# Kernel tuning notes

Measured on AMD Instinct MI355X. Metric: run time of the kernel, lower is better.

## Reference

```python
import jax, jax.numpy as jnp
import numpy as np

B, N, E = 4, 160, 200000
D_EDGE, D_ORI, D_TYPE = 128, 8, 120      # d_edge, d_ori_edge, d_edge_type = d_edge - d_ori_edge
D_EXT = 512                               # d_edge * expansion_factor(4)
D_H4 = 512                                # d_edge * 4
D_REL = 16
PML, ETN = 32, 16                         # path_max_length, edge_type_num


def setup_inputs() -> dict:
    key = jax.random.key(0)
    ks = jax.random.split(key, 16)
    p = lambda i, shape, s=0.05: (jax.random.normal(ks[i], shape) * s).astype(jnp.float32)
    return dict(
        rel_type=jax.random.randint(ks[0], (E,), 0, ETN),
        rel_error=jax.random.normal(ks[1], (E, D_ORI), jnp.float32),
        edge_pos=jax.random.randint(ks[2], (E,), 0, PML),
        dist=jax.random.randint(ks[3], (B, N, N), 0, PML),
        rel_row=jnp.sort(jax.random.randint(ks[4], (E,), 0, B * N * N)),
        rel_col=jax.random.randint(ks[5], (E,), 0, 10000),
        batch_num=B, max_node=N,
        type_tab=p(6, (ETN, D_TYPE), 1.0),
        pos_tab=p(7, (PML, D_EDGE), 1.0),
        dist_tab=p(8, (PML, D_EXT), 1.0),
        w1=p(9, (D_EDGE, 2 * D_EDGE)), b1=jnp.zeros(2 * D_EDGE, jnp.float32),
        w2=p(10, (2 * D_EDGE, 4 * D_EDGE)), b2=jnp.zeros(4 * D_EDGE, jnp.float32),
        w3=p(11, (4 * D_EDGE, D_EXT)), b3=jnp.zeros(D_EXT, jnp.float32),
        g1=jnp.ones(D_EXT, jnp.float32), be1=jnp.zeros(D_EXT, jnp.float32),
        wf1=p(12, (D_EXT, D_H4)), bf1=jnp.zeros(D_H4, jnp.float32),
        g2=jnp.ones(D_H4, jnp.float32), be2=jnp.zeros(D_H4, jnp.float32),
        wf2=p(13, (D_H4, D_H4)), bf2=jnp.zeros(D_H4, jnp.float32),
        g3=jnp.ones(D_H4, jnp.float32), be3=jnp.zeros(D_H4, jnp.float32),
        wf3=p(14, (D_H4, D_REL)), bf3=jnp.zeros(D_REL, jnp.float32),
    )


def _ln(x, g, b, eps=1e-5):
    m = x.mean(-1, keepdims=True)
    v = ((x - m) ** 2).mean(-1, keepdims=True)
    return (x - m) * jax.lax.rsqrt(v + eps) * g + b


def reference(rel_type, rel_error, edge_pos, dist, rel_row, rel_col, batch_num, max_node,
              type_tab, pos_tab, dist_tab,
              w1, b1, w2, b2, w3, b3,
              g1, be1, wf1, bf1, g2, be2, wf2, bf2, g3, be3, wf3, bf3):
    type_tab = type_tab.at[0].set(0.0)   # padding_idx=0
    dist_tab = dist_tab.at[0].set(0.0)   # padding_idx=0
    # embed + concat + positional add  -> [E, D_EDGE]
    e = jnp.concatenate([type_tab[rel_type], rel_error], axis=1) + pos_tab[edge_pos]
    # point-net style edge MLP -> [E, D_EXT]
    h = jax.nn.relu(e @ w1 + b1)
    h = jax.nn.relu(h @ w2 + b2)
    h = h @ w3 + b3
    # sparse scatter-max over the hybrid-COO row index (torch_sparse.reduce.max, dim=1)
    n_seg = batch_num * max_node * max_node
    seg = jax.ops.segment_max(h, rel_row, num_segments=n_seg, indices_are_sorted=True)
    seg = jnp.where(jnp.isneginf(seg), 0.0, seg)   # empty rows -> 0 (torch_scatter fill)
    rel = seg.reshape(batch_num, max_node, max_node, -1) + dist_tab[dist]
    # fc: ReLU, LN, Linear, ReLU, LN, Linear, ReLU, LN, Linear
    x = _ln(jax.nn.relu(rel), g1, be1) @ wf1 + bf1
    x = _ln(jax.nn.relu(x), g2, be2) @ wf2 + bf2
    x = _ln(jax.nn.relu(x), g3, be3) @ wf3 + bf3   # [B, N, N, D_REL]
    # triu over the (N, N) dims, then symmetrize
    mask = jnp.triu(jnp.ones((max_node, max_node), x.dtype))
    x = x * mask[None, :, :, None]
    return x + x.transpose(0, 2, 1, 3)
```

## Files before the change

kernel.cpp:

```cpp
#include <hip/hip_runtime.h>

typedef __attribute__((ext_vector_type(8))) _Float16 half8;
typedef __attribute__((ext_vector_type(4))) _Float16 half4;
typedef __attribute__((ext_vector_type(4))) float f32x4;

constexpr int Bn = 4;
constexpr int Nn = 160;
constexpr int SEGN = Bn * Nn * Nn;
constexpr int TRIN = Nn * (Nn + 1) / 2;
constexpr int CMPN = Bn * TRIN;
constexpr int SCAN_NB = (SEGN + 511) / 512;

__device__ __forceinline__ int tri_base(int i) { return i * Nn - (i * (i - 1)) / 2; }

__global__ void k_prep(const float* __restrict__ w1, const float* __restrict__ w2,
                       const float* __restrict__ w3, const float* __restrict__ wf1,
                       const float* __restrict__ wf2, const float* __restrict__ wf3,
                       _Float16* __restrict__ o1, _Float16* __restrict__ o2,
                       _Float16* __restrict__ o3, _Float16* __restrict__ of1,
                       _Float16* __restrict__ of2, _Float16* __restrict__ of3) {
  int t = blockIdx.x * 256 + threadIdx.x;
  const float* src; _Float16* dst; int N, local; bool is3 = false;
  if (t < 32768)       { src = w1;  dst = o1;  N = 256; local = t; }
  else if (t < 163840) { src = w2;  dst = o2;  N = 512; local = t - 32768; }
  else if (t < 425984) { src = w3;  dst = o3;  N = 512; local = t - 163840; }
  else if (t < 688128) { src = wf1; dst = of1; N = 512; local = t - 425984; }
  else if (t < 950272) { src = wf2; dst = of2; N = 512; local = t - 688128; }
  else if (t < 958464) { src = wf3; dst = of3; N = 16;  local = t - 950272; is3 = true; }
  else return;
  int k = local / N;
  int n = local - k * N;
  if (is3) dst[n * 512 + k] = (_Float16)src[local];
  else dst[(size_t)((k >> 5) * N + n) * 32 + (k & 31)] = (_Float16)src[local];
}

__device__ __forceinline__ int lower_bound_rr(const int* __restrict__ rel_row, int E, int key) {
  int lo = 0, hi = E;
  while (lo < hi) { int mid = (lo + hi) >> 1; if (rel_row[mid] < key) lo = mid + 1; else hi = mid; }
  return lo;
}

__global__ void k_cnt(const int* __restrict__ rel_row, int* __restrict__ row_ptr,
                      int* __restrict__ cnt, int* __restrict__ tri2ij, int E) {
  int r = blockIdx.x * 256 + threadIdx.x;
  if (r < TRIN) {
    int lo = 0, hi = Nn - 1;
    while (lo < hi) { int mid = (lo + hi + 1) >> 1; if (tri_base(mid) <= r) lo = mid; else hi = mid - 1; }
    int j = lo + (r - tri_base(lo));
    tri2ij[r] = (lo << 16) | j;
  }
  if (r > SEGN) return;
  int lo = lower_bound_rr(rel_row, E, r);
  row_ptr[r] = lo;
  if (r < SEGN) {
    int hi2 = lower_bound_rr(rel_row, E, r + 1);
    int jj = r % Nn;
    int ii = (r / Nn) % Nn;
    cnt[r] = (ii <= jj) ? (hi2 - lo) : 0;
  }
}

__global__ void k_scan1(const int* __restrict__ cnt, int* __restrict__ pre,
                        int* __restrict__ bsum) {
  __shared__ int tmp[512];
  int t = threadIdx.x, b = blockIdx.x;
  int idx = b * 512 + t;
  int v = (idx < SEGN) ? cnt[idx] : 0;
  tmp[t] = v;
  __syncthreads();
  for (int o = 1; o < 512; o <<= 1) {
    int add = (t >= o) ? tmp[t - o] : 0;
    __syncthreads();
    tmp[t] += add;
    __syncthreads();
  }
  if (idx < SEGN) pre[idx] = tmp[t] - v;
  if (t == 511) bsum[b] = tmp[511];
}

__global__ void k_scan2(int* __restrict__ bsum, int* __restrict__ ek) {
  __shared__ int tmp[256];
  int t = threadIdx.x;
  int v = (t < SCAN_NB) ? bsum[t] : 0;
  tmp[t] = v;
  __syncthreads();
  for (int o = 1; o < 256; o <<= 1) {
    int add = (t >= o) ? tmp[t - o] : 0;
    __syncthreads();
    tmp[t] += add;
    __syncthreads();
  }
  if (t < SCAN_NB) bsum[t] = tmp[t] - v;
  if (t == 255) ek[0] = tmp[255];
}

__global__ void k_map(const int* __restrict__ row_ptr, const int* __restrict__ cnt,
                      const int* __restrict__ pre, const int* __restrict__ bsum,
                      int* __restrict__ cstart, int* __restrict__ edge_map) {
  int r = blockIdx.x * 512 + threadIdx.x;
  if (r >= SEGN) return;
  int cs = pre[r] + bsum[r >> 9];
  cstart[r] = cs;
  int c = cnt[r];
  int rp = row_ptr[r];
  for (int k = 0; k < c; ++k) edge_map[cs + k] = rp + k;
  if (r == SEGN - 1) cstart[SEGN] = cs + c;
}

template <int MT, int K, int C0, int CN, int NSTRIDE, int NT, bool SP>
__device__ __forceinline__ void do_slice(const _Float16* __restrict__ wt,
                                         const char* a_base, int nbase,
                                         f32x4 (&acc)[MT][NT], int tid) {
  constexpr int rowB = K * 2;
  const int w = tid >> 6, lane = tid & 63, ln15 = lane & 15, kg = lane >> 4;
  const char* wb = (const char*)wt;
#pragma unroll
  for (int c = 0; c < CN; ++c) {
    half8 a[MT], b[NT];
#pragma unroll
    for (int nt = 0; nt < NT; ++nt) {
      int n = nbase + (w * NT + nt) * 16 + ln15;
      b[nt] = *(const half8*)(wb + (size_t)(C0 + c) * (NSTRIDE * 64) + n * 64 + kg * 16);
    }
#pragma unroll
    for (int mt = 0; mt < MT; ++mt) {
      int row = mt * 16 + ln15;
      int byte = (row * rowB + c * 64 + kg * 16) ^ ((row & 7) << 4);
      a[mt] = *(const half8*)(a_base + byte);
    }
    if (SP) __builtin_amdgcn_s_setprio(1);
#pragma unroll
    for (int mt = 0; mt < MT; ++mt)
#pragma unroll
      for (int nt = 0; nt < NT; ++nt)
        acc[mt][nt] = __builtin_amdgcn_mfma_f32_16x16x32_f16(a[mt], b[nt], acc[mt][nt], 0, 0, 0);
    if (SP) __builtin_amdgcn_s_setprio(0);
  }
}

template <int MT, int NT>
__device__ __forceinline__ void init_accn(const float* __restrict__ bias, int nbase,
                                          f32x4 (&acc)[MT][NT], int tid) {
  const int w = tid >> 6, ln15 = tid & 15;
#pragma unroll
  for (int nt = 0; nt < NT; ++nt) {
    float bv = bias[nbase + (w * NT + nt) * 16 + ln15];
    f32x4 s = {bv, bv, bv, bv};
#pragma unroll
    for (int mt = 0; mt < MT; ++mt) acc[mt][nt] = s;
  }
}

template <int MT, int NT, bool RELU>
__device__ __forceinline__ void store_hn(char* h, int rowB, int nbase,
                                         const f32x4 (&acc)[MT][NT], int tid) {
  const int w = tid >> 6, lane = tid & 63, ln15 = lane & 15, kg = lane >> 4;
#pragma unroll
  for (int mt = 0; mt < MT; ++mt)
#pragma unroll
    for (int nt = 0; nt < NT; ++nt)
#pragma unroll
      for (int j = 0; j < 4; ++j) {
        int row = mt * 16 + kg * 4 + j;
        int n = nbase + (w * NT + nt) * 16 + ln15;
        float v = acc[mt][nt][j];
        if (RELU) v = fmaxf(v, 0.f);
        *(_Float16*)(h + ((row * rowB + n * 2) ^ ((row & 7) << 4))) = (_Float16)v;
      }
}

__global__ __launch_bounds__(512) void k_edge(
    const int* __restrict__ rel_type, const float* __restrict__ rel_error,
    const int* __restrict__ edge_pos, const int* __restrict__ edge_map,
    const int* __restrict__ ekp,
    const float* __restrict__ type_tab, const float* __restrict__ pos_tab,
    const _Float16* __restrict__ w1t, const float* __restrict__ b1,
    const _Float16* __restrict__ w2t, const float* __restrict__ b2,
    const _Float16* __restrict__ w3t, const float* __restrict__ b3,
    _Float16* __restrict__ h3) {
  __shared__ __align__(16) char smem[98304];
  char* h1 = smem;
  char* h2 = smem + 32768;
  char* e  = smem + 32768;

  const int tid = threadIdx.x;
  const int e0 = blockIdx.x * 64;
  const int EK = ekp[0];
  if (e0 >= EK) return;

  {
    int r = tid >> 3, c0 = (tid & 7) * 16;
    int re = edge_map[min(e0 + r, EK - 1)];
    int rt = rel_type[re];
    int ep = edge_pos[re];
#pragma unroll
    for (int s = 0; s < 2; ++s) {
      half8 hv;
#pragma unroll
      for (int q = 0; q < 8; ++q) {
        int cc = c0 + s * 8 + q;
        float v = (cc < 120) ? (rt ? type_tab[rt * 120 + cc] : 0.f)
                             : rel_error[(size_t)re * 8 + (cc - 120)];
        v += pos_tab[ep * 128 + cc];
        hv[q] = (_Float16)v;
      }
      int byte = (r * 256 + (c0 + s * 8) * 2) ^ ((r & 7) << 4);
      *(half8*)(e + byte) = hv;
    }
  }
  __syncthreads();

  {
    f32x4 acc[4][2];
    init_accn<4, 2>(b1, 0, acc, tid);
    do_slice<4, 128, 0, 4, 256, 2, true>(w1t, e, 0, acc, tid);
    store_hn<4, 2, true>(h1, 512, 0, acc, tid);
  }
  __syncthreads();
  {
    f32x4 acc[4][4];
    init_accn<4, 4>(b2, 0, acc, tid);
    do_slice<4, 256, 0, 8, 512, 4, true>(w2t, h1, 0, acc, tid);
    store_hn<4, 4, true>(h2, 1024, 0, acc, tid);
  }
  __syncthreads();
  {
    f32x4 acc[4][4];
    init_accn<4, 4>(b3, 0, acc, tid);
    do_slice<4, 512, 0, 16, 512, 4, true>(w3t, h2, 0, acc, tid);
    __syncthreads();
    store_hn<4, 4, false>(h2, 1024, 0, acc, tid);
    __syncthreads();
    uint4* dst = (uint4*)(h3 + (size_t)e0 * 512);
#pragma unroll
    for (int i = 0; i < 8; ++i) {
      int cidx = tid + i * 512;
      int byteoff = cidx * 16;
      int row = byteoff >> 10;
      uint4 v = *(const uint4*)(h2 + (byteoff ^ ((row & 7) << 4)));
      if (e0 + row < EK) dst[cidx] = v;
    }
  }
}

__device__ __forceinline__ void epi_ln_store(f32x4 (&acc)[4][4], char* dst,
                                             float* st1, float* st2,
                                             float* stM, float* stR,
                                             const float* __restrict__ g,
                                             const float* __restrict__ be, int tid) {
  const int w = tid >> 6, lane = tid & 63, ln15 = lane & 15, kg = lane >> 4;
#pragma unroll
  for (int mt = 0; mt < 4; ++mt)
#pragma unroll
    for (int nt = 0; nt < 4; ++nt)
#pragma unroll
      for (int j = 0; j < 4; ++j) acc[mt][nt][j] = fmaxf(acc[mt][nt][j], 0.f);
#pragma unroll
  for (int mt = 0; mt < 4; ++mt)
#pragma unroll
    for (int j = 0; j < 4; ++j) {
      float a = 0.f, b = 0.f;
#pragma unroll
      for (int nt = 0; nt < 4; ++nt) { float v = acc[mt][nt][j]; a += v; b += v * v; }
#pragma unroll
      for (int m = 1; m < 16; m <<= 1) { a += __shfl_xor(a, m); b += __shfl_xor(b, m); }
      if (ln15 == 0) {
        int r = mt * 16 + kg * 4 + j;
        st1[w * 64 + r] = a;
        st2[w * 64 + r] = b;
      }
    }
  __syncthreads();
  if (tid < 64) {
    float a = 0.f, b = 0.f;
#pragma unroll
    for (int ww = 0; ww < 8; ++ww) { a += st1[ww * 64 + tid]; b += st2[ww * 64 + tid]; }
    float mean = a * (1.f / 512.f);
    float var = b * (1.f / 512.f) - mean * mean;
    stM[tid] = mean;
    stR[tid] = rsqrtf(var + 1e-5f);
  }
  __syncthreads();
  float gv[4], bv[4];
#pragma unroll
  for (int nt = 0; nt < 4; ++nt) {
    int n = (w * 4 + nt) * 16 + ln15;
    gv[nt] = g[n]; bv[nt] = be[n];
  }
#pragma unroll
  for (int mt = 0; mt < 4; ++mt)
#pragma unroll
    for (int j = 0; j < 4; ++j) {
      int r = mt * 16 + kg * 4 + j;
      float mean = stM[r], rs = stR[r];
#pragma unroll
      for (int nt = 0; nt < 4; ++nt) {
        int n = (w * 4 + nt) * 16 + ln15;
        float v = (acc[mt][nt][j] - mean) * rs * gv[nt] + bv[nt];
        *(_Float16*)(dst + ((r * 1024 + n * 2) ^ ((r & 7) << 4))) = (_Float16)v;
      }
    }
  __syncthreads();
}

__global__ __launch_bounds__(512, 2) void k_fc(
    const _Float16* __restrict__ h3, const int* __restrict__ cstart,
    const int* __restrict__ tri2ij,
    const int* __restrict__ dist, const float* __restrict__ dist_tab,
    const float* __restrict__ g1, const float* __restrict__ be1,
    const _Float16* __restrict__ wf1t, const float* __restrict__ bf1,
    const float* __restrict__ g2, const float* __restrict__ be2,
    const _Float16* __restrict__ wf2t, const float* __restrict__ bf2,
    const float* __restrict__ g3, const float* __restrict__ be3,
    const _Float16* __restrict__ wf3t, const float* __restrict__ bf3,
    float* __restrict__ x3c) {
  __shared__ __align__(16) char bufA[65536];
  __shared__ float st1[512], st2[512];
  __shared__ float stM[64], stR[64];

  const int tid = threadIdx.x;
  const int p0 = blockIdx.x * 64;

  {
    const int w = tid >> 6, lane = tid & 63;
    const int coff = lane * 8;
    const float* gp = g1 + coff;
    const float* bp = be1 + coff;
    const _Float16 NEGH = (_Float16)(-65504.f);
    for (int rr = 0; rr < 8; ++rr) {
      int rloc = w * 8 + rr;
      int p = p0 + rloc;
      int b = p / TRIN;
      int ij = tri2ij[p - b * TRIN];
      int gr = (b * Nn + (ij >> 16)) * Nn + (ij & 0xffff);
      int s = cstart[gr], en = cstart[gr + 1];
      int di = dist[gr];
      half8 mx;
#pragma unroll
      for (int q = 0; q < 8; ++q) mx[q] = NEGH;
      int idx = s;
      while (idx + 4 <= en) {
        half8 c0 = *(const half8*)(h3 + (size_t)(idx + 0) * 512 + coff);
        half8 c1 = *(const half8*)(h3 + (size_t)(idx + 1) * 512 + coff);
        half8 c2 = *(const half8*)(h3 + (size_t)(idx + 2) * 512 + coff);
        half8 c3 = *(const half8*)(h3 + (size_t)(idx + 3) * 512 + coff);
        mx = __builtin_elementwise_max(mx, __builtin_elementwise_max(
                 __builtin_elementwise_max(c0, c1), __builtin_elementwise_max(c2, c3)));
        idx += 4;
      }
      if (idx + 2 <= en) {
        half8 c0 = *(const half8*)(h3 + (size_t)(idx + 0) * 512 + coff);
        half8 c1 = *(const half8*)(h3 + (size_t)(idx + 1) * 512 + coff);
        mx = __builtin_elementwise_max(mx, __builtin_elementwise_max(c0, c1));
        idx += 2;
      }
      if (idx < en) {
        half8 c0 = *(const half8*)(h3 + (size_t)idx * 512 + coff);
        mx = __builtin_elementwise_max(mx, c0);
      }
      const float* dt = dist_tab + (size_t)di * 512 + coff;
      float v[8]; float s1 = 0.f, s2 = 0.f;
#pragma unroll
      for (int q = 0; q < 8; ++q) {
        float vv = (s == en) ? 0.f : (float)mx[q];
        if (di) vv += dt[q];
        vv = fmaxf(vv, 0.f);
        v[q] = vv; s1 += vv; s2 += vv * vv;
      }
#pragma unroll
      for (int o = 32; o > 0; o >>= 1) { s1 += __shfl_xor(s1, o); s2 += __shfl_xor(s2, o); }
      float mean = s1 * (1.f / 512.f);
      float rs = rsqrtf(s2 * (1.f / 512.f) - mean * mean + 1e-5f);
      half8 ov;
#pragma unroll
      for (int q = 0; q < 8; ++q) ov[q] = (_Float16)((v[q] - mean) * rs * gp[q] + bp[q]);
      *(half8*)(bufA + ((rloc * 1024 + coff * 2) ^ ((rloc & 7) << 4))) = ov;
    }
  }
  __syncthreads();

  {
    f32x4 acc[4][4];
    init_accn<4, 4>(bf1, 0, acc, tid);
    do_slice<4, 512, 0, 16, 512, 4, true>(wf1t, bufA, 0, acc, tid);
    epi_ln_store(acc, bufA, st1, st2, stM, stR, g2, be2, tid);
  }
  {
    f32x4 acc[4][4];
    init_accn<4, 4>(bf2, 0, acc, tid);
    do_slice<4, 512, 0, 16, 512, 4, true>(wf2t, bufA, 0, acc, tid);
    epi_ln_store(acc, bufA, st1, st2, stM, stR, g3, be3, tid);
  }
  {
    const int w = tid >> 6, lane = tid & 63, ln15 = lane & 15, kg = lane >> 4;
    if (w < 4) {
      f32x4 acc3 = {0.f, 0.f, 0.f, 0.f};
#pragma unroll
      for (int c = 0; c < 16; ++c) {
        half8 b = *(const half8*)((const char*)wf3t + ln15 * 1024 + c * 64 + kg * 16);
        int row = w * 16 + ln15;
        half8 a = *(const half8*)(bufA + ((row * 1024 + c * 64 + kg * 16) ^ ((row & 7) << 4)));
        acc3 = __builtin_amdgcn_mfma_f32_16x16x32_f16(a, b, acc3, 0, 0, 0);
      }
#pragma unroll
      for (int j = 0; j < 4; ++j)
        x3c[(size_t)(p0 + w * 16 + kg * 4 + j) * 16 + ln15] = acc3[j] + bf3[ln15];
    }
  }
}

__global__ void k_sym(const float* __restrict__ x3c, float* __restrict__ out) {
  int t = blockIdx.x * 256 + threadIdx.x;
  if (t >= SEGN * 4) return;
  int q = t & 3;
  int cell = t >> 2;
  int j = cell % Nn;
  int tmp = cell / Nn;
  int i = tmp % Nn;
  int b = tmp / Nn;
  int lo = min(i, j), hi = i ^ j ^ lo;
  int p = b * TRIN + tri_base(lo) + (hi - lo);
  float4 v = *(const float4*)&x3c[(size_t)p * 16 + q * 4];
  if (i == j) { v.x *= 2.f; v.y *= 2.f; v.z *= 2.f; v.w *= 2.f; }
  *(float4*)&out[(size_t)t * 4] = v;
}

extern "C" void kernel_launch(void* const* d_in, const int* in_sizes, int n_in,
                              void* d_out, int out_size, void* d_ws, size_t ws_size,
                              hipStream_t stream) {
  const int*   rel_type  = (const int*)d_in[0];
  const float* rel_error = (const float*)d_in[1];
  const int*   edge_pos  = (const int*)d_in[2];
  const int*   dist      = (const int*)d_in[3];
  const int*   rel_row   = (const int*)d_in[4];
  const float* type_tab = (const float*)d_in[8];
  const float* pos_tab  = (const float*)d_in[9];
  const float* dist_tab = (const float*)d_in[10];
  const float* w1 = (const float*)d_in[11]; const float* b1 = (const float*)d_in[12];
  const float* w2 = (const float*)d_in[13]; const float* b2 = (const float*)d_in[14];
  const float* w3 = (const float*)d_in[15]; const float* b3 = (const float*)d_in[16];
  const float* g1 = (const float*)d_in[17]; const float* be1 = (const float*)d_in[18];
  const float* wf1 = (const float*)d_in[19]; const float* bf1 = (const float*)d_in[20];
  const float* g2 = (const float*)d_in[21]; const float* be2 = (const float*)d_in[22];
  const float* wf2 = (const float*)d_in[23]; const float* bf2 = (const float*)d_in[24];
  const float* g3 = (const float*)d_in[25]; const float* be3 = (const float*)d_in[26];
  const float* wf3 = (const float*)d_in[27]; const float* bf3 = (const float*)d_in[28];

  const int E = in_sizes[0];
  const size_t h3_bytes   = (size_t)E * 512 * 2;
  const size_t x3_bytes   = (size_t)CMPN * 16 * 4;
  const size_t ptr_bytes  = (size_t)(SEGN + 1) * 4;
  const size_t tri_bytes  = (size_t)TRIN * 4;
  const size_t cell_bytes = (size_t)SEGN * 4;
  const size_t cst_bytes  = (size_t)(SEGN + 1) * 4;
  const size_t map_bytes  = (size_t)E * 4;
  const size_t wt_elems   = 32768 + 131072 + 262144 * 3 + 8192;
  const size_t total = h3_bytes + x3_bytes + ptr_bytes + tri_bytes + 2 * cell_bytes +
                       cst_bytes + map_bytes + 1024 + 256 * 4 + wt_elems * 2;
  if (ws_size < total) return;

  char* wp = (char*)d_ws;
  _Float16* h3      = (_Float16*)wp;            wp += h3_bytes;
  float*    x3c     = (float*)wp;               wp += x3_bytes;
  int*      row_ptr = (int*)wp;                 wp += ptr_bytes;
  int*      tri2ij  = (int*)wp;                 wp += tri_bytes;
  int*      cnt     = (int*)wp;                 wp += cell_bytes;
  int*      pre     = (int*)wp;                 wp += cell_bytes;
  int*      cstart  = (int*)wp;                 wp += cst_bytes;
  int*      edge_map= (int*)wp;                 wp += map_bytes;
  int*      bsum    = (int*)wp;                 wp += 256 * 4;
  int*      ekp     = (int*)wp;                 wp += 1024;
  _Float16* w1t     = (_Float16*)wp;
  _Float16* w2t  = w1t + 32768;
  _Float16* w3t  = w2t + 131072;
  _Float16* wf1t = w3t + 262144;
  _Float16* wf2t = wf1t + 262144;
  _Float16* wf3t = wf2t + 262144;
  float*    out  = (float*)d_out;

  k_prep<<<3744, 256, 0, stream>>>(w1, w2, w3, wf1, wf2, wf3,
                                   w1t, w2t, w3t, wf1t, wf2t, wf3t);
  k_cnt<<<(SEGN + 256) / 256, 256, 0, stream>>>(rel_row, row_ptr, cnt, tri2ij, E);
  k_scan1<<<SCAN_NB, 512, 0, stream>>>(cnt, pre, bsum);
  k_scan2<<<1, 256, 0, stream>>>(bsum, ekp);
  k_map<<<SCAN_NB, 512, 0, stream>>>(row_ptr, cnt, pre, bsum, cstart, edge_map);
  k_edge<<<(E + 63) / 64, 512, 0, stream>>>(rel_type, rel_error, edge_pos, edge_map, ekp,
                                            type_tab, pos_tab, w1t, b1, w2t, b2, w3t, b3,
                                            h3);
  k_fc<<<CMPN / 64, 512, 0, stream>>>(h3, cstart, tri2ij, dist, dist_tab,
                                      g1, be1, wf1t, bf1,
                                      g2, be2, wf2t, bf2,
                                      g3, be3, wf3t, bf3, x3c);
  k_sym<<<(SEGN * 4 + 255) / 256, 256, 0, stream>>>(x3c, out);
}
```

Baseline: 389.3 us.

## Split sparse max-gather and first LayerNorm out of fused FC kernel

```diff
diff --git a/kernel.cpp b/kernel.cpp
--- a/kernel.cpp
+++ b/kernel.cpp
@@ -243,6 +243,69 @@
   }
 }
 
+__global__ __launch_bounds__(256) void k_gather(
+    const _Float16* __restrict__ h3, const int* __restrict__ cstart,
+    const int* __restrict__ tri2ij, const int* __restrict__ dist,
+    const float* __restrict__ dist_tab,
+    const float* __restrict__ g1, const float* __restrict__ be1,
+    _Float16* __restrict__ rowsA) {
+  const int w = threadIdx.x >> 6, lane = threadIdx.x & 63;
+  const int coff = lane * 8;
+  const float* gp = g1 + coff;
+  const float* bp = be1 + coff;
+  const _Float16 NEGH = (_Float16)(-65504.f);
+  const int pbase = blockIdx.x * 32 + w * 8;
+  for (int rr = 0; rr < 8; ++rr) {
+    int p = pbase + rr;
+    if (p >= CMPN) return;
+    int b = p / TRIN;
+    int ij = tri2ij[p - b * TRIN];
+    int gr = (b * Nn + (ij >> 16)) * Nn + (ij & 0xffff);
+    int s = cstart[gr], en = cstart[gr + 1];
+    int di = dist[gr];
+    half8 mx;
+#pragma unroll
+    for (int q = 0; q < 8; ++q) mx[q] = NEGH;
+    int idx = s;
+    while (idx + 4 <= en) {
+      half8 c0 = *(const half8*)(h3 + (size_t)(idx + 0) * 512 + coff);
+      half8 c1 = *(const half8*)(h3 + (size_t)(idx + 1) * 512 + coff);
+      half8 c2 = *(const half8*)(h3 + (size_t)(idx + 2) * 512 + coff);
+      half8 c3 = *(const half8*)(h3 + (size_t)(idx + 3) * 512 + coff);
+      mx = __builtin_elementwise_max(mx, __builtin_elementwise_max(
+               __builtin_elementwise_max(c0, c1), __builtin_elementwise_max(c2, c3)));
+      idx += 4;
+    }
+    if (idx + 2 <= en) {
+      half8 c0 = *(const half8*)(h3 + (size_t)(idx + 0) * 512 + coff);
+      half8 c1 = *(const half8*)(h3 + (size_t)(idx + 1) * 512 + coff);
+      mx = __builtin_elementwise_max(mx, __builtin_elementwise_max(c0, c1));
+      idx += 2;
+    }
+    if (idx < en) {
+      half8 c0 = *(const half8*)(h3 + (size_t)idx * 512 + coff);
+      mx = __builtin_elementwise_max(mx, c0);
+    }
+    const float* dt = dist_tab + (size_t)di * 512 + coff;
+    float v[8]; float s1 = 0.f, s2 = 0.f;
+#pragma unroll
+    for (int q = 0; q < 8; ++q) {
+      float vv = (s == en) ? 0.f : (float)mx[q];
+      if (di) vv += dt[q];
+      vv = fmaxf(vv, 0.f);
+      v[q] = vv; s1 += vv; s2 += vv * vv;
+    }
+#pragma unroll
+    for (int o = 32; o > 0; o >>= 1) { s1 += __shfl_xor(s1, o); s2 += __shfl_xor(s2, o); }
+    float mean = s1 * (1.f / 512.f);
+    float rs = rsqrtf(s2 * (1.f / 512.f) - mean * mean + 1e-5f);
+    half8 ov;
+#pragma unroll
+    for (int q = 0; q < 8; ++q) ov[q] = (_Float16)((v[q] - mean) * rs * gp[q] + bp[q]);
+    *(half8*)((char*)rowsA + (size_t)p * 1024 + ((coff * 2) ^ ((p & 7) << 4))) = ov;
+  }
+}
+
 __device__ __forceinline__ void epi_ln_store(f32x4 (&acc)[4][4], char* dst,
                                              float* st1, float* st2,
                                              float* stM, float* stR,
@@ -303,15 +366,12 @@
   __syncthreads();
 }
 
-__global__ __launch_bounds__(512, 2) void k_fc(
-    const _Float16* __restrict__ h3, const int* __restrict__ cstart,
-    const int* __restrict__ tri2ij,
-    const int* __restrict__ dist, const float* __restrict__ dist_tab,
-    const float* __restrict__ g1, const float* __restrict__ be1,
+__global__ __launch_bounds__(512, 2) void k_fcg(
+    const _Float16* __restrict__ rowsA,
+    const float* __restrict__ g2, const float* __restrict__ be2,
     const _Float16* __restrict__ wf1t, const float* __restrict__ bf1,
-    const float* __restrict__ g2, const float* __restrict__ be2,
+    const float* __restrict__ g3, const float* __restrict__ be3,
     const _Float16* __restrict__ wf2t, const float* __restrict__ bf2,
-    const float* __restrict__ g3, const float* __restrict__ be3,
     const _Float16* __restrict__ wf3t, const float* __restrict__ bf3,
     float* __restrict__ x3c) {
   __shared__ __align__(16) char bufA[65536];
@@ -322,60 +382,10 @@
   const int p0 = blockIdx.x * 64;
 
   {
-    const int w = tid >> 6, lane = tid & 63;
-    const int coff = lane * 8;
-    const float* gp = g1 + coff;
-    const float* bp = be1 + coff;
-    const _Float16 NEGH = (_Float16)(-65504.f);
-    for (int rr = 0; rr < 8; ++rr) {
-      int rloc = w * 8 + rr;
-      int p = p0 + rloc;
-      int b = p / TRIN;
-      int ij = tri2ij[p - b * TRIN];
-      int gr = (b * Nn + (ij >> 16)) * Nn + (ij & 0xffff);
-      int s = cstart[gr], en = cstart[gr + 1];
-      int di = dist[gr];
-      half8 mx;
-#pragma unroll
-      for (int q = 0; q < 8; ++q) mx[q] = NEGH;
-      int idx = s;
-      while (idx + 4 <= en) {
-        half8 c0 = *(const half8*)(h3 + (size_t)(idx + 0) * 512 + coff);
-        half8 c1 = *(const half8*)(h3 + (size_t)(idx + 1) * 512 + coff);
-        half8 c2 = *(const half8*)(h3 + (size_t)(idx + 2) * 512 + coff);
-        half8 c3 = *(const half8*)(h3 + (size_t)(idx + 3) * 512 + coff);
-        mx = __builtin_elementwise_max(mx, __builtin_elementwise_max(
-                 __builtin_elementwise_max(c0, c1), __builtin_elementwise_max(c2, c3)));
-        idx += 4;
-      }
-      if (idx + 2 <= en) {
-        half8 c0 = *(const half8*)(h3 + (size_t)(idx + 0) * 512 + coff);
-        half8 c1 = *(const half8*)(h3 + (size_t)(idx + 1) * 512 + coff);
-        mx = __builtin_elementwise_max(mx, __builtin_elementwise_max(c0, c1));
-        idx += 2;
-      }
-      if (idx < en) {
-        half8 c0 = *(const half8*)(h3 + (size_t)idx * 512 + coff);
-        mx = __builtin_elementwise_max(mx, c0);
-      }
-      const float* dt = dist_tab + (size_t)di * 512 + coff;
-      float v[8]; float s1 = 0.f, s2 = 0.f;
-#pragma unroll
-      for (int q = 0; q < 8; ++q) {
-        float vv = (s == en) ? 0.f : (float)mx[q];
-        if (di) vv += dt[q];
-        vv = fmaxf(vv, 0.f);
-        v[q] = vv; s1 += vv; s2 += vv * vv;
-      }
-#pragma unroll
-      for (int o = 32; o > 0; o >>= 1) { s1 += __shfl_xor(s1, o); s2 += __shfl_xor(s2, o); }
-      float mean = s1 * (1.f / 512.f);
-      float rs = rsqrtf(s2 * (1.f / 512.f) - mean * mean + 1e-5f);
-      half8 ov;
-#pragma unroll
-      for (int q = 0; q < 8; ++q) ov[q] = (_Float16)((v[q] - mean) * rs * gp[q] + bp[q]);
-      *(half8*)(bufA + ((rloc * 1024 + coff * 2) ^ ((rloc & 7) << 4))) = ov;
-    }
+    const uint4* src = (const uint4*)((const char*)rowsA + (size_t)p0 * 1024);
+    uint4* dst = (uint4*)bufA;
+#pragma unroll
+    for (int i = 0; i < 8; ++i) dst[tid + i * 512] = src[tid + i * 512];
   }
   __syncthreads();
 
@@ -448,6 +458,7 @@
 
   const int E = in_sizes[0];
   const size_t h3_bytes   = (size_t)E * 512 * 2;
+  const size_t rows_off   = ((size_t)E * 55 / 100) * 1024;
   const size_t x3_bytes   = (size_t)CMPN * 16 * 4;
   const size_t ptr_bytes  = (size_t)(SEGN + 1) * 4;
   const size_t tri_bytes  = (size_t)TRIN * 4;
@@ -460,7 +471,9 @@
   if (ws_size < total) return;
 
   char* wp = (char*)d_ws;
-  _Float16* h3      = (_Float16*)wp;            wp += h3_bytes;
+  _Float16* h3      = (_Float16*)wp;
+  _Float16* rowsA   = (_Float16*)(wp + rows_off);
+  wp += h3_bytes;
   float*    x3c     = (float*)wp;               wp += x3_bytes;
   int*      row_ptr = (int*)wp;                 wp += ptr_bytes;
   int*      tri2ij  = (int*)wp;                 wp += tri_bytes;
@@ -487,9 +500,11 @@
   k_edge<<<(E + 63) / 64, 512, 0, stream>>>(rel_type, rel_error, edge_pos, edge_map, ekp,
                                             type_tab, pos_tab, w1t, b1, w2t, b2, w3t, b3,
                                             h3);
-  k_fc<<<CMPN / 64, 512, 0, stream>>>(h3, cstart, tri2ij, dist, dist_tab,
-                                      g1, be1, wf1t, bf1,
-                                      g2, be2, wf2t, bf2,
-                                      g3, be3, wf3t, bf3, x3c);
+  k_gather<<<(CMPN + 31) / 32, 256, 0, stream>>>(h3, cstart, tri2ij, dist, dist_tab,
+                                                 g1, be1, rowsA);
+  k_fcg<<<CMPN / 64, 512, 0, stream>>>(rowsA,
+                                       g2, be2, wf1t, bf1,
+                                       g3, be3, wf2t, bf2,
+                                       wf3t, bf3, x3c);
   k_sym<<<(SEGN * 4 + 255) / 256, 256, 0, stream>>>(x3c, out);
 }
```

Result: faster. 375.4 us (-3.6%).
